# Kernel tuning notes

Measured on AMD Instinct MI355X. Metric: run time of the kernel, lower is better.

Reference implementation:

```python
import jax, jax.numpy as jnp
import numpy as np

RADIUS = 0.4   # 0.2 * nlayer, nlayer = 2
NSAMPLE = 32   # k


def _fps(xyz, m):
    """Farthest point sampling. xyz: (B, N, 3) -> idx (B, m) int32.
    Matches pointnet2 CUDA kernel: first sampled point is index 0."""
    B, N, _ = xyz.shape

    def step(carry, _):
        dist, far = carry
        centroid = jnp.take_along_axis(xyz, far[:, None, None], axis=1)  # (B,1,3)
        d = jnp.sum((xyz - centroid) ** 2, axis=-1)                      # (B,N)
        dist = jnp.minimum(dist, d)
        return (dist, jnp.argmax(dist, axis=-1).astype(jnp.int32)), far

    init = (jnp.full((B, N), jnp.inf, dtype=xyz.dtype),
            jnp.zeros((B,), dtype=jnp.int32))
    _, idx = jax.lax.scan(step, init, None, length=m)  # (m, B)
    return idx.T                                       # (B, m)


def _ball_query(radius, k, xyz, new_xyz):
    """xyz (B,N,3), new_xyz (B,M,3) -> (B,M,k) int32.
    First k in-radius indices in ascending index order; slots past the
    number of in-radius points are filled with the first found index
    (pointnet2 ball_query semantics)."""
    N = xyz.shape[1]
    d2 = jnp.sum((new_xyz[:, :, None, :] - xyz[:, None, :, :]) ** 2, axis=-1)  # (B,M,N)
    key = jnp.where(d2 < radius * radius,
                    jnp.arange(N, dtype=jnp.int32), jnp.int32(N))              # (B,M,N)
    topv, _ = jax.lax.top_k(-key, k)   # k smallest keys, ascending
    idx = -topv                        # (B,M,k)
    valid = idx < N
    idx = jnp.where(valid, idx, idx[..., :1])  # pad with first found index
    return idx


def _group(t, idx):
    """t (B,C,N), idx (B,M,k) -> (B,C,M,k)."""
    return jnp.take_along_axis(t[:, :, None, :], idx[:, None, :, :], axis=3)


def setup_inputs() -> dict:
    key = jax.random.key(0)
    k1, k2, k3 = jax.random.split(key, 3)
    return {
        "x": jax.random.normal(k1, (8, 3, 8192), dtype=jnp.float32),
        "feature": jax.random.normal(k2, (8, 64, 8192), dtype=jnp.float32),
        "weight": jax.random.normal(k3, (64, 64), dtype=jnp.float32) / 8.0,
        "num_pool": 2048,
    }


def reference(x, feature, weight, num_pool):
    # x: (B,3,N) coordinates, feature: (B,C,N), weight: 1x1 conv (C_out, C_in)
    xyz = jnp.transpose(x, (0, 2, 1))                       # (B,N,3)
    fps_idx = _fps(xyz, num_pool)                           # (B,M)
    new_xyz = jnp.take_along_axis(xyz, fps_idx[:, :, None], axis=1)  # (B,M,3)
    sub_idx = _ball_query(RADIUS, NSAMPLE, xyz, new_xyz)    # (B,M,k)

    x_out = _group(x, sub_idx).max(axis=-1)                 # (B,3,M)
    fg = _group(feature, sub_idx)                           # (B,C,M,k)
    f_out = jnp.einsum('oc,bcmk->bomk', weight, fg).max(axis=-1)  # (B,C,M)
    return x_out, f_out
```

## Files before the change

### kernel.cpp

```cpp
#include <hip/hip_runtime.h>
#include <cstdint>
#include <cstddef>

#define BB 8
#define NN 8192
#define CC 64
#define MM 2048
#define KK 32

typedef float vfloat2 __attribute__((ext_vector_type(2)));

__device__ __forceinline__ float sqdist_exact(float x, float y, float z,
                                              float cx, float cy, float cz) {
    float dx = __fsub_rn(x, cx);
    float dy = __fsub_rn(y, cy);
    float dz = __fsub_rn(z, cz);
    return __fadd_rn(__fadd_rn(__fmul_rn(dx, dx), __fmul_rn(dy, dy)),
                     __fmul_rn(dz, dz));
}

template <int CTRL>
__device__ __forceinline__ unsigned dpp_max_u32(unsigned v) {
    unsigned s = (unsigned)__builtin_amdgcn_update_dpp(0, (int)v, CTRL, 0xF, 0xF, true);
    return v > s ? v : s;
}
template <int CTRL>
__device__ __forceinline__ unsigned dpp_min_u32(unsigned v) {
    unsigned s = (unsigned)__builtin_amdgcn_update_dpp(0x7FFFFFFF, (int)v, CTRL, 0xF, 0xF, false);
    return v < s ? v : s;
}

__device__ __forceinline__ int octile(float v) {
    return (v > -1.1503494f) + (v > -0.6744898f) + (v > -0.3186394f) + (v > 0.0f) +
           (v > 0.3186394f) + (v > 0.6744898f) + (v > 1.1503494f);
}

__device__ __forceinline__ int morton9(int bx, int by, int bz) {
    int m = (bz & 1) | ((bz & 2) << 2) | ((bz & 4) << 4);
    m |= ((by & 1) << 1) | ((by & 2) << 3) | ((by & 4) << 5);
    m |= ((bx & 1) << 2) | ((bx & 2) << 4) | ((bx & 4) << 6);
    return m;
}

__global__ __launch_bounds__(512) void fps_kernel(const float* __restrict__ x,
                                                  int* __restrict__ fps_idx) {
#pragma clang fp contract(off)
    const int b = blockIdx.x;
    const int tid = threadIdx.x;
    const int lane = tid & 63;
    const int wv = tid >> 6;
    const float* xb = x + (size_t)b * 3 * NN;
    int* fps_store = fps_idx + b * MM;

    __shared__ float sx[NN];
    __shared__ float sy[NN];
    __shared__ float sz[NN];
    __shared__ int sidx[NN];
    __shared__ int hist[512];
    __shared__ int scanb[512];
    __shared__ int sfps[MM];
    __shared__ unsigned long long red2[2][8];

    const vfloat2* gx = (const vfloat2*)xb;
    const vfloat2* gy = (const vfloat2*)(xb + NN);
    const vfloat2* gz = (const vfloat2*)(xb + 2 * NN);

    vfloat2 lx[8], ly[8], lz[8];
#pragma unroll
    for (int p = 0; p < 8; ++p) {
        const int e = tid + p * 512;
        lx[p] = gx[e];
        ly[p] = gy[e];
        lz[p] = gz[e];
        ((vfloat2*)sx)[e] = lx[p];
        ((vfloat2*)sy)[e] = ly[p];
        ((vfloat2*)sz)[e] = lz[p];
    }
    hist[tid] = 0;
    __syncthreads();

    int mybin[16];
#pragma unroll
    for (int p = 0; p < 8; ++p) {
        int b0 = morton9(octile(lx[p].x), octile(ly[p].x), octile(lz[p].x));
        int b1 = morton9(octile(lx[p].y), octile(ly[p].y), octile(lz[p].y));
        mybin[2 * p] = b0;
        mybin[2 * p + 1] = b1;
        atomicAdd(&hist[b0], 1);
        atomicAdd(&hist[b1], 1);
    }
    __syncthreads();
    int own = hist[tid];
    scanb[tid] = own;
    __syncthreads();
    for (int off = 1; off < 512; off <<= 1) {
        int add = (tid >= off) ? scanb[tid - off] : 0;
        __syncthreads();
        scanb[tid] += add;
        __syncthreads();
    }
    hist[tid] = scanb[tid] - own;
    __syncthreads();
#pragma unroll
    for (int p = 0; p < 8; ++p) {
        const int i0 = 2 * (tid + p * 512);
        int pos0 = atomicAdd(&hist[mybin[2 * p]], 1);
        sidx[pos0] = i0;
        int pos1 = atomicAdd(&hist[mybin[2 * p + 1]], 1);
        sidx[pos1] = i0 + 1;
    }
    __syncthreads();

    float px[16], py[16], pz[16], dist[16];
    int idxr[16];
#pragma unroll
    for (int p = 0; p < 16; ++p) {
        const int j = sidx[tid * 16 + p];
        idxr[p] = j;
        px[p] = sx[j];
        py[p] = sy[j];
        pz[p] = sz[j];
        dist[p] = INFINITY;
    }
    float blx = px[0], bhx = px[0];
    float bly = py[0], bhy = py[0];
    float blz = pz[0], bhz = pz[0];
#pragma unroll
    for (int p = 1; p < 16; ++p) {
        blx = fminf(blx, px[p]); bhx = fmaxf(bhx, px[p]);
        bly = fminf(bly, py[p]); bhy = fmaxf(bhy, py[p]);
        blz = fminf(blz, pz[p]); bhz = fmaxf(bhz, pz[p]);
    }

    float cmax = INFINITY;
    int cidx = idxr[0];
    int far = 0;
    for (int t = 0; t < MM; ++t) {
        if (tid == 0) sfps[t] = far;
        const float cx = sx[far];
        const float cy = sy[far];
        const float cz = sz[far];

        float qx = cx - fminf(fmaxf(cx, blx), bhx);
        float qy = cy - fminf(fmaxf(cy, bly), bhy);
        float qz = cz - fminf(fmaxf(cz, blz), bhz);
        float bound = (qx * qx + qy * qy) + qz * qz;
        if (!(bound * 0.999f >= cmax)) {
            float mv = -1.0f;
#pragma unroll
            for (int p = 0; p < 16; ++p) {
                float dx = px[p] - cx;
                float dy = py[p] - cy;
                float dz = pz[p] - cz;
                float s = (dx * dx + dy * dy) + dz * dz;
                float nd = fminf(dist[p], s);
                dist[p] = nd;
                mv = fmaxf(mv, nd);
            }
            int mi = 0x7FFFFFFF;
#pragma unroll
            for (int p = 0; p < 16; ++p) {
                int cand = (dist[p] == mv) ? idxr[p] : 0x7FFFFFFF;
                mi = min(mi, cand);
            }
            cmax = mv;
            cidx = mi;
        }

        unsigned mvb = __float_as_uint(cmax);
        mvb = dpp_max_u32<0x111>(mvb);
        mvb = dpp_max_u32<0x112>(mvb);
        mvb = dpp_max_u32<0x114>(mvb);
        mvb = dpp_max_u32<0x118>(mvb);
        mvb = dpp_max_u32<0x142>(mvb);
        mvb = dpp_max_u32<0x143>(mvb);
        const unsigned wmax = (unsigned)__builtin_amdgcn_readlane((int)mvb, 63);
        unsigned midx = (__float_as_uint(cmax) == wmax) ? (unsigned)cidx : 0x7FFFFFFFu;
        midx = dpp_min_u32<0x111>(midx);
        midx = dpp_min_u32<0x112>(midx);
        midx = dpp_min_u32<0x114>(midx);
        midx = dpp_min_u32<0x118>(midx);
        midx = dpp_min_u32<0x142>(midx);
        midx = dpp_min_u32<0x143>(midx);
        if (lane == 63) {
            red2[t & 1][wv] =
                ((unsigned long long)wmax << 32) | (unsigned)(~midx);
        }
        __syncthreads();
        const unsigned long long* r = red2[t & 1];
        unsigned long long k0 = r[0], k1 = r[1], k2 = r[2], k3 = r[3];
        unsigned long long k4 = r[4], k5 = r[5], k6 = r[6], k7 = r[7];
        unsigned long long a0 = k0 > k1 ? k0 : k1;
        unsigned long long a1 = k2 > k3 ? k2 : k3;
        unsigned long long a2 = k4 > k5 ? k4 : k5;
        unsigned long long a3 = k6 > k7 ? k6 : k7;
        unsigned long long b0 = a0 > a1 ? a0 : a1;
        unsigned long long b1 = a2 > a3 ? a2 : a3;
        unsigned long long best = b0 > b1 ? b0 : b1;
        far = (int)(~(unsigned)best);
    }
    __syncthreads();
    for (int t = tid; t < MM; t += 512) fps_store[t] = sfps[t];
}

__global__ __launch_bounds__(256) void transform_kernel(const float* __restrict__ feature,
                                                        const float* __restrict__ weight,
                                                        float* __restrict__ g) {
    __shared__ float Wl[64 * 64];
    const int tid = threadIdx.x;
    for (int k = tid; k < 64 * 64; k += 256) Wl[k] = weight[k];
    __syncthreads();

    const int P = blockIdx.x * 256 + tid;
    const int b = P >> 13;
    const int n = P & (NN - 1);
    const float* fb = feature + (size_t)b * CC * NN + n;

    float fr[64];
#pragma unroll
    for (int c = 0; c < 64; ++c) fr[c] = fb[(size_t)c * NN];

    float* go = g + ((size_t)b << 19) + (size_t)n * 64;
    for (int o = 0; o < 64; o += 4) {
        const float* w0 = &Wl[o * 64];
        const float* w1 = w0 + 64;
        const float* w2 = w0 + 128;
        const float* w3 = w0 + 192;
        float a0 = 0.f, a1 = 0.f, a2 = 0.f, a3 = 0.f;
#pragma unroll
        for (int c = 0; c < 64; c += 4) {
            float4 v0 = *(const float4*)(w0 + c);
            float4 v1 = *(const float4*)(w1 + c);
            float4 v2 = *(const float4*)(w2 + c);
            float4 v3 = *(const float4*)(w3 + c);
            a0 += v0.x * fr[c] + v0.y * fr[c + 1] + v0.z * fr[c + 2] + v0.w * fr[c + 3];
            a1 += v1.x * fr[c] + v1.y * fr[c + 1] + v1.z * fr[c + 2] + v1.w * fr[c + 3];
            a2 += v2.x * fr[c] + v2.y * fr[c + 1] + v2.z * fr[c + 2] + v2.w * fr[c + 3];
            a3 += v3.x * fr[c] + v3.y * fr[c + 1] + v3.z * fr[c + 2] + v3.w * fr[c + 3];
        }
        float4 r;
        r.x = a0; r.y = a1; r.z = a2; r.w = a3;
        *(float4*)(go + o) = r;
    }
}

__global__ __launch_bounds__(256) void bq_kernel(const float* __restrict__ x,
                                                 const int* __restrict__ fps_idx,
                                                 int* __restrict__ sub_idx,
                                                 float* __restrict__ xout) {
    const float R2 = (float)(0.4 * 0.4);
    int gw = (int)((blockIdx.x * 256 + threadIdx.x) >> 6);
    const int lane = threadIdx.x & 63;
    gw = __builtin_amdgcn_readfirstlane(gw);
    const int b = gw >> 11;
    const int m = gw & (MM - 1);
    const float* xb = x + (size_t)b * 3 * NN;

    const int ctr = fps_idx[gw];
    const float cx = xb[ctr];
    const float cy = xb[NN + ctr];
    const float cz = xb[2 * NN + ctr];

    int* sid = sub_idx + (size_t)gw * KK;
    int found = 0;
    int first = 0;
    float mx = -INFINITY, my = -INFINITY, mz = -INFINITY;

    for (int base = 0; base < NN; base += 64) {
        const int i = base + lane;
        const float xx = xb[i];
        const float yy = xb[NN + i];
        const float zz = xb[2 * NN + i];
        const float d2 = sqdist_exact(xx, yy, zz, cx, cy, cz);
        const bool q = d2 < R2;
        const unsigned long long mask = __ballot(q);
        if (q) {
            int pos = found + (int)__popcll(mask & ((1ull << lane) - 1ull));
            if (pos < KK) {
                sid[pos] = i;
                mx = fmaxf(mx, xx);
                my = fmaxf(my, yy);
                mz = fmaxf(mz, zz);
            }
        }
        if (found == 0 && mask != 0ull) first = base + (int)__builtin_ctzll(mask);
        found += (int)__popcll(mask);
        if (found >= KK) break;
    }
    if (found < KK) {
        if (lane < KK - found) sid[found + lane] = first;
    }
#pragma unroll
    for (int off = 32; off >= 1; off >>= 1) {
        mx = fmaxf(mx, __shfl_xor(mx, off, 64));
        my = fmaxf(my, __shfl_xor(my, off, 64));
        mz = fmaxf(mz, __shfl_xor(mz, off, 64));
    }
    if (lane == 0) {
        xout[(size_t)b * 3 * MM + 0 * MM + m] = mx;
        xout[(size_t)b * 3 * MM + 1 * MM + m] = my;
        xout[(size_t)b * 3 * MM + 2 * MM + m] = mz;
    }
}

__global__ __launch_bounds__(256) void gather_kernel(const float* __restrict__ g,
                                                     const int* __restrict__ sub_idx,
                                                     float* __restrict__ fout) {
    int gw = (int)((blockIdx.x * 256 + threadIdx.x) >> 6);
    const int lane = threadIdx.x & 63;
    gw = __builtin_amdgcn_readfirstlane(gw);
    const int b = gw >> 11;
    const int m = gw & (MM - 1);
    const int* sid = sub_idx + (size_t)gw * KK;
    const float* gb = g + ((size_t)b << 19);
    float acc = -INFINITY;
#pragma unroll
    for (int j = 0; j < KK; ++j) {
        const int id = sid[j];
        acc = fmaxf(acc, gb[(size_t)id * 64 + lane]);
    }
    fout[((size_t)b << 17) + ((size_t)lane << 11) + m] = acc;
}

extern "C" void kernel_launch(void* const* d_in, const int* in_sizes, int n_in,
                              void* d_out, int out_size, void* d_ws, size_t ws_size,
                              hipStream_t stream) {
    const float* x = (const float*)d_in[0];
    const float* feature = (const float*)d_in[1];
    const float* weight = (const float*)d_in[2];

    float* out = (float*)d_out;
    float* xout = out;
    float* fout = out + BB * 3 * MM;

    char* ws = (char*)d_ws;
    int* fps_idx = (int*)ws;
    int* sub_idx = (int*)(ws + (size_t)BB * MM * 4);
    float* g = (float*)(ws + (size_t)BB * MM * 4 + (size_t)BB * MM * KK * 4);

    fps_kernel<<<BB, 512, 0, stream>>>(x, fps_idx);
    transform_kernel<<<(BB * NN) / 256, 256, 0, stream>>>(feature, weight, g);
    bq_kernel<<<(BB * MM * 64) / 256, 256, 0, stream>>>(x, fps_idx, sub_idx, xout);
    gather_kernel<<<(BB * MM * 64) / 256, 256, 0, stream>>>(g, sub_idx, fout);
}
```

Measured before the change: 1.933 ms.

## Pack FPS distance updates into float2 and skip wave reduction when idle

Stores each thread's 16 points as eight float2 vectors so subtract and multiply can use packed FP32 instructions. Adds a wave-level ballot so that when no lane in a wave needs to update its distances, the whole wave skips both the distance loop and the DPP max/argmin reduction, reusing its cached per-wave key. This cuts per-iteration latency in the serial FPS loop. The trade-off is extra register pressure and a ballot on every iteration.

Measured after the change: 2.275 ms. +17.7%, slower.

```diff
diff --git a/kernel.cpp b/kernel.cpp
--- a/kernel.cpp
+++ b/kernel.cpp
@@ -111,29 +111,35 @@
     }
     __syncthreads();
 
-    float px[16], py[16], pz[16], dist[16];
+    vfloat2 px[8], py[8], pz[8], dist[8];
     int idxr[16];
 #pragma unroll
-    for (int p = 0; p < 16; ++p) {
-        const int j = sidx[tid * 16 + p];
-        idxr[p] = j;
-        px[p] = sx[j];
-        py[p] = sy[j];
-        pz[p] = sz[j];
-        dist[p] = INFINITY;
-    }
-    float blx = px[0], bhx = px[0];
-    float bly = py[0], bhy = py[0];
-    float blz = pz[0], bhz = pz[0];
-#pragma unroll
-    for (int p = 1; p < 16; ++p) {
-        blx = fminf(blx, px[p]); bhx = fmaxf(bhx, px[p]);
-        bly = fminf(bly, py[p]); bhy = fmaxf(bhy, py[p]);
-        blz = fminf(blz, pz[p]); bhz = fmaxf(bhz, pz[p]);
+    for (int p = 0; p < 8; ++p) {
+        const int j0 = sidx[tid * 16 + 2 * p];
+        const int j1 = sidx[tid * 16 + 2 * p + 1];
+        idxr[2 * p] = j0;
+        idxr[2 * p + 1] = j1;
+        px[p] = (vfloat2){sx[j0], sx[j1]};
+        py[p] = (vfloat2){sy[j0], sy[j1]};
+        pz[p] = (vfloat2){sz[j0], sz[j1]};
+        dist[p] = (vfloat2){INFINITY, INFINITY};
+    }
+    float blx = fminf(px[0].x, px[0].y), bhx = fmaxf(px[0].x, px[0].y);
+    float bly = fminf(py[0].x, py[0].y), bhy = fmaxf(py[0].x, py[0].y);
+    float blz = fminf(pz[0].x, pz[0].y), bhz = fmaxf(pz[0].x, pz[0].y);
+#pragma unroll
+    for (int p = 1; p < 8; ++p) {
+        blx = fminf(blx, fminf(px[p].x, px[p].y));
+        bhx = fmaxf(bhx, fmaxf(px[p].x, px[p].y));
+        bly = fminf(bly, fminf(py[p].x, py[p].y));
+        bhy = fmaxf(bhy, fmaxf(py[p].x, py[p].y));
+        blz = fminf(blz, fminf(pz[p].x, pz[p].y));
+        bhz = fmaxf(bhz, fmaxf(pz[p].x, pz[p].y));
     }
 
     float cmax = INFINITY;
     int cidx = idxr[0];
+    unsigned long long wkey = 0;
     int far = 0;
     for (int t = 0; t < MM; ++t) {
         if (tid == 0) sfps[t] = far;
@@ -145,47 +151,55 @@
         float qy = cy - fminf(fmaxf(cy, bly), bhy);
         float qz = cz - fminf(fmaxf(cz, blz), bhz);
         float bound = (qx * qx + qy * qy) + qz * qz;
-        if (!(bound * 0.999f >= cmax)) {
-            float mv = -1.0f;
-#pragma unroll
-            for (int p = 0; p < 16; ++p) {
-                float dx = px[p] - cx;
-                float dy = py[p] - cy;
-                float dz = pz[p] - cz;
-                float s = (dx * dx + dy * dy) + dz * dz;
-                float nd = fminf(dist[p], s);
-                dist[p] = nd;
-                mv = fmaxf(mv, nd);
+        const bool act = !(bound * 0.999f >= cmax);
+        if (__ballot(act) != 0ull) {
+            if (act) {
+                const vfloat2 cx2 = {cx, cx};
+                const vfloat2 cy2 = {cy, cy};
+                const vfloat2 cz2 = {cz, cz};
+                float mv = -1.0f;
+#pragma unroll
+                for (int p = 0; p < 8; ++p) {
+                    vfloat2 dx = px[p] - cx2;
+                    vfloat2 dy = py[p] - cy2;
+                    vfloat2 dz = pz[p] - cz2;
+                    vfloat2 m1 = dx * dx;
+                    vfloat2 m2 = dy * dy;
+                    vfloat2 m3 = dz * dz;
+                    vfloat2 s = (m1 + m2) + m3;
+                    vfloat2 nd;
+                    nd.x = fminf(dist[p].x, s.x);
+                    nd.y = fminf(dist[p].y, s.y);
+                    dist[p] = nd;
+                    mv = fmaxf(fmaxf(mv, nd.x), nd.y);
+                }
+                int mi = 0x7FFFFFFF;
+#pragma unroll
+                for (int p = 0; p < 8; ++p) {
+                    mi = min(mi, (dist[p].x == mv) ? idxr[2 * p] : 0x7FFFFFFF);
+                    mi = min(mi, (dist[p].y == mv) ? idxr[2 * p + 1] : 0x7FFFFFFF);
+                }
+                cmax = mv;
+                cidx = mi;
             }
-            int mi = 0x7FFFFFFF;
-#pragma unroll
-            for (int p = 0; p < 16; ++p) {
-                int cand = (dist[p] == mv) ? idxr[p] : 0x7FFFFFFF;
-                mi = min(mi, cand);
-            }
-            cmax = mv;
-            cidx = mi;
+            unsigned mvb = __float_as_uint(cmax);
+            mvb = dpp_max_u32<0x111>(mvb);
+            mvb = dpp_max_u32<0x112>(mvb);
+            mvb = dpp_max_u32<0x114>(mvb);
+            mvb = dpp_max_u32<0x118>(mvb);
+            mvb = dpp_max_u32<0x142>(mvb);
+            mvb = dpp_max_u32<0x143>(mvb);
+            const unsigned wmax = (unsigned)__builtin_amdgcn_readlane((int)mvb, 63);
+            unsigned midx = (__float_as_uint(cmax) == wmax) ? (unsigned)cidx : 0x7FFFFFFFu;
+            midx = dpp_min_u32<0x111>(midx);
+            midx = dpp_min_u32<0x112>(midx);
+            midx = dpp_min_u32<0x114>(midx);
+            midx = dpp_min_u32<0x118>(midx);
+            midx = dpp_min_u32<0x142>(midx);
+            midx = dpp_min_u32<0x143>(midx);
+            wkey = ((unsigned long long)wmax << 32) | (unsigned)(~midx);
         }
-
-        unsigned mvb = __float_as_uint(cmax);
-        mvb = dpp_max_u32<0x111>(mvb);
-        mvb = dpp_max_u32<0x112>(mvb);
-        mvb = dpp_max_u32<0x114>(mvb);
-        mvb = dpp_max_u32<0x118>(mvb);
-        mvb = dpp_max_u32<0x142>(mvb);
-        mvb = dpp_max_u32<0x143>(mvb);
-        const unsigned wmax = (unsigned)__builtin_amdgcn_readlane((int)mvb, 63);
-        unsigned midx = (__float_as_uint(cmax) == wmax) ? (unsigned)cidx : 0x7FFFFFFFu;
-        midx = dpp_min_u32<0x111>(midx);
-        midx = dpp_min_u32<0x112>(midx);
-        midx = dpp_min_u32<0x114>(midx);
-        midx = dpp_min_u32<0x118>(midx);
-        midx = dpp_min_u32<0x142>(midx);
-        midx = dpp_min_u32<0x143>(midx);
-        if (lane == 63) {
-            red2[t & 1][wv] =
-                ((unsigned long long)wmax << 32) | (unsigned)(~midx);
-        }
+        if (lane == 63) red2[t & 1][wv] = wkey;
         __syncthreads();
         const unsigned long long* r = red2[t & 1];
         unsigned long long k0 = r[0], k1 = r[1], k2 = r[2], k3 = r[3];
```
